# Kernel tuning notes

Measured on AMD Instinct MI355X. Metric: run time of the kernel, lower is better.

The kernel has to match this reference:

```python
import jax, jax.numpy as jnp
import numpy as np

N_GRAPHS = 64
EPS = 1e-5

def setup_inputs() -> dict:
    key = jax.random.key(0)
    ks = jax.random.split(key, 5)
    N, E, F_IN, F_OUT = 50000, 800000, 64, 64
    x = jax.random.normal(ks[0], (N, F_IN), dtype=jnp.float32)
    W = jax.random.normal(ks[1], (F_IN, F_OUT), dtype=jnp.float32) * (1.0 / np.sqrt(F_IN))
    b = jnp.zeros((F_OUT,), dtype=jnp.float32)
    gn_weight = jnp.ones((F_OUT,), dtype=jnp.float32)
    gn_bias = jnp.zeros((F_OUT,), dtype=jnp.float32)
    gn_mean_scale = jnp.ones((F_OUT,), dtype=jnp.float32)
    edge_index = jax.random.randint(ks[2], (2, E), 0, N, dtype=jnp.int64)
    batch = jnp.sort(jax.random.randint(ks[3], (N,), 0, N_GRAPHS, dtype=jnp.int64))
    return {"x": x, "W": W, "b": b, "gn_weight": gn_weight, "gn_bias": gn_bias,
            "gn_mean_scale": gn_mean_scale, "edge_index": edge_index, "batch": batch}

def reference(x, W, b, gn_weight, gn_bias, gn_mean_scale, edge_index, batch):
    N = x.shape[0]
    # --- GCNConv: add self-loops, symmetric degree normalization ---
    loop = jnp.arange(N, dtype=edge_index.dtype)
    src = jnp.concatenate([edge_index[0], loop])  # message sources (x_j)
    dst = jnp.concatenate([edge_index[1], loop])  # aggregation targets
    h = x @ W                                      # [N, F_out]
    deg = jax.ops.segment_sum(jnp.ones_like(dst, dtype=h.dtype), dst, num_segments=N)
    dinv = jnp.where(deg > 0, jax.lax.rsqrt(deg), 0.0)
    norm = dinv[src] * dinv[dst]                   # [E+N]
    out = jax.ops.segment_sum(norm[:, None] * h[src], dst, num_segments=N) + b
    # --- GraphNorm: per-graph mean/var with learnable mean scale ---
    ones = jnp.ones((N,), dtype=out.dtype)
    cnt = jax.ops.segment_sum(ones, batch, num_segments=N_GRAPHS)[:, None]  # [G,1]
    mean = jax.ops.segment_sum(out, batch, num_segments=N_GRAPHS) / cnt     # [G,F]
    centered = out - gn_mean_scale * mean[batch]
    var = jax.ops.segment_sum(centered * centered, batch, num_segments=N_GRAPHS) / cnt
    normed = centered * jax.lax.rsqrt(var[batch] + EPS)
    return jax.nn.relu(gn_weight * normed + gn_bias)
```

## Files before the change

kernel.cpp:

```cpp
#include <hip/hip_runtime.h>
#include <stdint.h>

#define EPS 1e-5f
#define NG 64
#define NP 8
#define MSLOT 64
#define CH 128

typedef float f32x4 __attribute__((ext_vector_type(4)));
typedef __bf16 bf16x8 __attribute__((ext_vector_type(8)));
typedef unsigned short u16x8 __attribute__((ext_vector_type(8)));

__device__ __forceinline__ unsigned short f2bf(float f) {
    union { float f; uint32_t u; } v; v.f = f;
    uint32_t r = v.u + 0x7fff + ((v.u >> 16) & 1);
    return (unsigned short)(r >> 16);
}
__device__ __forceinline__ float bflo(uint32_t u) {
    union { uint32_t u; float f; } v; v.u = u << 16; return v.f;
}
__device__ __forceinline__ float bfhi(uint32_t u) {
    union { uint32_t u; float f; } v; v.u = u & 0xffff0000u; return v.f;
}

__global__ __launch_bounds__(256) void setup(const float* __restrict__ W,
                                             unsigned short* __restrict__ wf,
                                             int* __restrict__ rowpos, int N,
                                             int* __restrict__ zbase, int zcount) {
    int i = blockIdx.x * 256 + threadIdx.x;
    if (i < N) rowpos[i] = i << 6;
    if (i < zcount) zbase[i] = 0;
    if (blockIdx.x == 0) {
        for (int k = threadIdx.x; k < 512; k += 256) {
            int lane = k & 63;
            int c = k >> 7;
            int s = (k >> 6) & 1;
            int col = 16 * c + (lane & 15);
            int k0 = 32 * s + (lane >> 4) * 8;
#pragma unroll
            for (int j = 0; j < 8; ++j)
                wf[k * 8 + j] = f2bf(W[(k0 + j) * 64 + col]);
        }
    }
}

__global__ __launch_bounds__(256) void fill_xcd(const int* __restrict__ src,
                                                const int* __restrict__ dst,
                                                int* __restrict__ rowpos,
                                                unsigned short* __restrict__ csr2,
                                                int E, int N, int rng, int chunk) {
    int b = blockIdx.x;
    int p = b & (NP - 1);
    int lo = p * rng;
    int hi = min(lo + rng, N);
    int base = (b >> 3) * chunk;
    int end = min(base + chunk, E);
    for (int e = base + threadIdx.x; e < end; e += 256) {
        int d = dst[e];
        if (d >= lo && d < hi) {
            int pos = atomicAdd(&rowpos[d], 1);
            if (pos < (d << 6) + MSLOT)
                __builtin_nontemporal_store((unsigned short)src[e], &csr2[pos]);
        }
    }
}

__global__ __launch_bounds__(256) void gemm_mfma(const float* __restrict__ x,
                                                 const unsigned short* __restrict__ wf,
                                                 const int* __restrict__ rowpos,
                                                 unsigned short* __restrict__ hb, int N) {
    int w = threadIdx.x >> 6;
    int lane = threadIdx.x & 63;
    int rowbase = blockIdx.x * 64 + w * 16;

    bf16x8 bfrag[4][2];
#pragma unroll
    for (int c = 0; c < 4; ++c)
#pragma unroll
        for (int s = 0; s < 2; ++s) {
            u16x8 u = *reinterpret_cast<const u16x8*>(wf + ((c * 2 + s) * 64 + lane) * 8);
            bfrag[c][s] = __builtin_bit_cast(bf16x8, u);
        }

    int ar = rowbase + (lane & 15);
    int k0 = (lane >> 4) * 8;
    bf16x8 afrag[2];
#pragma unroll
    for (int s = 0; s < 2; ++s) {
        u16x8 u = {0, 0, 0, 0, 0, 0, 0, 0};
        if (ar < N) {
            const float* xp = x + (size_t)ar * 64 + 32 * s + k0;
#pragma unroll
            for (int j = 0; j < 8; ++j) u[j] = f2bf(xp[j]);
        }
        afrag[s] = __builtin_bit_cast(bf16x8, u);
    }

    f32x4 acc[4];
#pragma unroll
    for (int c = 0; c < 4; ++c) acc[c] = (f32x4){0.f, 0.f, 0.f, 0.f};
#pragma unroll
    for (int s = 0; s < 2; ++s)
#pragma unroll
        for (int c = 0; c < 4; ++c)
            acc[c] = __builtin_amdgcn_mfma_f32_16x16x32_bf16(afrag[s], bfrag[c][s], acc[c], 0, 0, 0);

    int r0 = rowbase + (lane >> 4) * 4;
    int col = lane & 15;
#pragma unroll
    for (int j = 0; j < 4; ++j) {
        int node = r0 + j;
        if (node < N) {
            int deg = rowpos[node] - (node << 6);
            float dd = rsqrtf(1.0f + (float)deg);
#pragma unroll
            for (int c = 0; c < 4; ++c)
                hb[(size_t)node * 64 + 16 * c + col] = f2bf(acc[c][j] * dd);
        }
    }
}

__global__ __launch_bounds__(256) void gather_conv(const int* __restrict__ rowpos,
                                                   const unsigned short* __restrict__ csr2,
                                                   const uint2* __restrict__ hb2,
                                                   const float* __restrict__ bia,
                                                   float* __restrict__ out, int N) {
    int nd = blockIdx.x * 16 + (threadIdx.x >> 4);
    if (nd >= N) return;
    int l = threadIdx.x & 15;
    int degf = rowpos[nd] - (nd << 6);
    int deg = min(degf, MSLOT);
    float dd = rsqrtf(1.0f + (float)degf);

    uint2 hv = hb2[(size_t)nd * 16 + l];
    float a0 = bflo(hv.x), a1 = bfhi(hv.x), a2 = bflo(hv.y), a3 = bfhi(hv.y);
    int s0 = nd << 6;
    int s1 = s0 + deg;
    int j = s0;
    for (; j + 4 <= s1; j += 4) {
        unsigned long long iq = *reinterpret_cast<const unsigned long long*>(csr2 + j);
        int i0 = (int)(iq & 0xffff), i1 = (int)((iq >> 16) & 0xffff);
        int i2 = (int)((iq >> 32) & 0xffff), i3 = (int)(iq >> 48);
        uint2 v0 = hb2[(size_t)i0 * 16 + l];
        uint2 v1 = hb2[(size_t)i1 * 16 + l];
        uint2 v2 = hb2[(size_t)i2 * 16 + l];
        uint2 v3 = hb2[(size_t)i3 * 16 + l];
        a0 += bflo(v0.x) + bflo(v1.x) + bflo(v2.x) + bflo(v3.x);
        a1 += bfhi(v0.x) + bfhi(v1.x) + bfhi(v2.x) + bfhi(v3.x);
        a2 += bflo(v0.y) + bflo(v1.y) + bflo(v2.y) + bflo(v3.y);
        a3 += bfhi(v0.y) + bfhi(v1.y) + bfhi(v2.y) + bfhi(v3.y);
    }
    for (; j < s1; ++j) {
        uint2 v = hb2[(size_t)csr2[j] * 16 + l];
        a0 += bflo(v.x);
        a1 += bfhi(v.x);
        a2 += bflo(v.y);
        a3 += bfhi(v.y);
    }
    float4 bb = *reinterpret_cast<const float4*>(bia + 4 * l);
    float4 r;
    r.x = bb.x + dd * a0;
    r.y = bb.y + dd * a1;
    r.z = bb.z + dd * a2;
    r.w = bb.w + dd * a3;
    *reinterpret_cast<float4*>(out + (size_t)nd * 64 + 4 * l) = r;
}

__global__ __launch_bounds__(256) void stats_partial(const float* __restrict__ out,
                                                     const int* __restrict__ batch,
                                                     float* __restrict__ macc,
                                                     float* __restrict__ vacc,
                                                     int* __restrict__ cntacc, int N) {
    int c0 = blockIdx.x * CH;
    int c1 = min(c0 + CH, N);
    if (c0 >= N) return;
    int t = threadIdx.x, col = t & 63, rg = t >> 6;
    __shared__ int bsh[CH];
    __shared__ float red[4][64], red2[4][64];
    for (int i = t; i < c1 - c0; i += 256) bsh[i] = batch[c0 + i];
    __syncthreads();
    int s = c0;
    while (s < c1) {
        int g = bsh[s - c0];
        int e = s + 1;
        while (e < c1 && bsh[e - c0] == g) ++e;
        float sum = 0.f, sq = 0.f;
        for (int r = s + rg; r < e; r += 4) {
            float v = out[(size_t)r * 64 + col];
            sum += v;
            sq += v * v;
        }
        red[rg][col] = sum;
        red2[rg][col] = sq;
        __syncthreads();
        if (t < 64) {
            atomicAdd(&macc[g * 64 + t], red[0][t] + red[1][t] + red[2][t] + red[3][t]);
            atomicAdd(&vacc[g * 64 + t], red2[0][t] + red2[1][t] + red2[2][t] + red2[3][t]);
        }
        if (t == 0) atomicAdd(&cntacc[g], e - s);
        __syncthreads();
        s = e;
    }
}

__global__ void gn_final(float* __restrict__ out, const int* __restrict__ batch,
                         const float* __restrict__ ms, const float* __restrict__ macc,
                         const float* __restrict__ vacc, const int* __restrict__ cntacc,
                         const float* __restrict__ gw, const float* __restrict__ gb,
                         int total4) {
    int idx = blockIdx.x * 256 + threadIdx.x;
    if (idx >= total4) return;
    int i = idx >> 4, q = idx & 15;
    int g = batch[i];
    float inv = 1.f / (float)max(cntacc[g], 1);
    float4 mv = *reinterpret_cast<const float4*>(macc + g * 64 + 4 * q);
    float4 vv = *reinterpret_cast<const float4*>(vacc + g * 64 + 4 * q);
    float4 msf = *reinterpret_cast<const float4*>(ms + 4 * q);
    float4 gwv = *reinterpret_cast<const float4*>(gw + 4 * q);
    float4 gbv = *reinterpret_cast<const float4*>(gb + 4 * q);
    float4 o = *reinterpret_cast<const float4*>(out + (size_t)i * 64 + 4 * q);
    float m, var, y;
    float4 res;
    m = mv.x * inv; var = vv.x * inv - m * m * msf.x * (2.f - msf.x);
    y = (o.x - msf.x * m) * rsqrtf(var + EPS); res.x = fmaxf(gwv.x * y + gbv.x, 0.f);
    m = mv.y * inv; var = vv.y * inv - m * m * msf.y * (2.f - msf.y);
    y = (o.y - msf.y * m) * rsqrtf(var + EPS); res.y = fmaxf(gwv.y * y + gbv.y, 0.f);
    m = mv.z * inv; var = vv.z * inv - m * m * msf.z * (2.f - msf.z);
    y = (o.z - msf.z * m) * rsqrtf(var + EPS); res.z = fmaxf(gwv.z * y + gbv.z, 0.f);
    m = mv.w * inv; var = vv.w * inv - m * m * msf.w * (2.f - msf.w);
    y = (o.w - msf.w * m) * rsqrtf(var + EPS); res.w = fmaxf(gwv.w * y + gbv.w, 0.f);
    *reinterpret_cast<float4*>(out + (size_t)i * 64 + 4 * q) = res;
}

extern "C" void kernel_launch(void* const* d_in, const int* in_sizes, int n_in,
                              void* d_out, int out_size, void* d_ws, size_t ws_size,
                              hipStream_t stream) {
    const float* x  = (const float*)d_in[0];
    const float* W  = (const float*)d_in[1];
    const float* b  = (const float*)d_in[2];
    const float* gw = (const float*)d_in[3];
    const float* gb = (const float*)d_in[4];
    const float* ms = (const float*)d_in[5];
    const int*   edge  = (const int*)d_in[6];
    const int*   batch = (const int*)d_in[7];

    int N = in_sizes[0] / 64;
    int E = in_sizes[6] / 2;
    const int* src = edge;
    const int* dst = edge + E;

    float* out = (float*)d_out;

    unsigned short* hb = (unsigned short*)d_ws;
    int*   rowpos    = (int*)(hb + (size_t)N * 64);
    float* macc      = (float*)(rowpos + N);
    float* vacc      = macc + 64 * 64;
    int*   cntacc    = (int*)(vacc + 64 * 64);
    unsigned short* csr2 = (unsigned short*)(cntacc + 80);
    unsigned short* wf   = csr2 + (size_t)N * MSLOT;

    int chunk = (E + 255) / 256;
    int rng = (N + NP - 1) / NP;
    int zcount = 2 * 64 * 64 + 80;
    int setup_n = max(N, zcount);

    setup<<<(setup_n + 255) / 256, 256, 0, stream>>>(W, wf, rowpos, N, (int*)macc, zcount);
    fill_xcd<<<2048, 256, 0, stream>>>(src, dst, rowpos, csr2, E, N, rng, chunk);
    gemm_mfma<<<(N + 63) / 64, 256, 0, stream>>>(x, wf, rowpos, hb, N);
    gather_conv<<<(N + 15) / 16, 256, 0, stream>>>(rowpos, csr2, (const uint2*)hb, b, out, N);
    stats_partial<<<(N + CH - 1) / CH, 256, 0, stream>>>(out, batch, macc, vacc, cntacc, N);
    gn_final<<<(N * 16 + 255) / 256, 256, 0, stream>>>(out, batch, ms, macc, vacc, cntacc,
                                                       gw, gb, N * 16);
}
```

Baseline: 103.0 us.

## Split bf16 feature table into two column halves and gather each separately

The GEMM output is now written as two separate bf16 tables, each holding 32 of the 64 feature columns. The gather kernel runs over a 2D grid where blockIdx.y picks a half, using 8 lanes per node instead of 16. Each half-table is half the size of the full table, so the random neighbor gathers should hit L2/MALL more often. The cost is that the CSR index lists and degree values are read twice, and twice as many half-width row gathers are issued.

```diff
diff --git a/kernel.cpp b/kernel.cpp
--- a/kernel.cpp
+++ b/kernel.cpp
@@ -68,7 +68,8 @@
 __global__ __launch_bounds__(256) void gemm_mfma(const float* __restrict__ x,
                                                  const unsigned short* __restrict__ wf,
                                                  const int* __restrict__ rowpos,
-                                                 unsigned short* __restrict__ hb, int N) {
+                                                 unsigned short* __restrict__ hbA,
+                                                 unsigned short* __restrict__ hbB, int N) {
     int w = threadIdx.x >> 6;
     int lane = threadIdx.x & 63;
     int rowbase = blockIdx.x * 64 + w * 16;
@@ -114,25 +115,31 @@
             int deg = rowpos[node] - (node << 6);
             float dd = rsqrtf(1.0f + (float)deg);
 #pragma unroll
-            for (int c = 0; c < 4; ++c)
-                hb[(size_t)node * 64 + 16 * c + col] = f2bf(acc[c][j] * dd);
-        }
-    }
-}
-
-__global__ __launch_bounds__(256) void gather_conv(const int* __restrict__ rowpos,
+            for (int c = 0; c < 4; ++c) {
+                unsigned short v = f2bf(acc[c][j] * dd);
+                if (c < 2) hbA[(size_t)node * 32 + 16 * c + col] = v;
+                else       hbB[(size_t)node * 32 + 16 * (c - 2) + col] = v;
+            }
+        }
+    }
+}
+
+__global__ __launch_bounds__(256) void gather_half(const int* __restrict__ rowpos,
                                                    const unsigned short* __restrict__ csr2,
-                                                   const uint2* __restrict__ hb2,
+                                                   const uint2* __restrict__ hA2,
+                                                   const uint2* __restrict__ hB2,
                                                    const float* __restrict__ bia,
                                                    float* __restrict__ out, int N) {
-    int nd = blockIdx.x * 16 + (threadIdx.x >> 4);
+    int half = blockIdx.y;
+    const uint2* hb2 = half ? hB2 : hA2;
+    int nd = blockIdx.x * 32 + (threadIdx.x >> 3);
     if (nd >= N) return;
-    int l = threadIdx.x & 15;
+    int l = threadIdx.x & 7;
     int degf = rowpos[nd] - (nd << 6);
     int deg = min(degf, MSLOT);
     float dd = rsqrtf(1.0f + (float)degf);
 
-    uint2 hv = hb2[(size_t)nd * 16 + l];
+    uint2 hv = hb2[(size_t)nd * 8 + l];
     float a0 = bflo(hv.x), a1 = bfhi(hv.x), a2 = bflo(hv.y), a3 = bfhi(hv.y);
     int s0 = nd << 6;
     int s1 = s0 + deg;
@@ -141,29 +148,30 @@
         unsigned long long iq = *reinterpret_cast<const unsigned long long*>(csr2 + j);
         int i0 = (int)(iq & 0xffff), i1 = (int)((iq >> 16) & 0xffff);
         int i2 = (int)((iq >> 32) & 0xffff), i3 = (int)(iq >> 48);
-        uint2 v0 = hb2[(size_t)i0 * 16 + l];
-        uint2 v1 = hb2[(size_t)i1 * 16 + l];
-        uint2 v2 = hb2[(size_t)i2 * 16 + l];
-        uint2 v3 = hb2[(size_t)i3 * 16 + l];
+        uint2 v0 = hb2[(size_t)i0 * 8 + l];
+        uint2 v1 = hb2[(size_t)i1 * 8 + l];
+        uint2 v2 = hb2[(size_t)i2 * 8 + l];
+        uint2 v3 = hb2[(size_t)i3 * 8 + l];
         a0 += bflo(v0.x) + bflo(v1.x) + bflo(v2.x) + bflo(v3.x);
         a1 += bfhi(v0.x) + bfhi(v1.x) + bfhi(v2.x) + bfhi(v3.x);
         a2 += bflo(v0.y) + bflo(v1.y) + bflo(v2.y) + bflo(v3.y);
         a3 += bfhi(v0.y) + bfhi(v1.y) + bfhi(v2.y) + bfhi(v3.y);
     }
     for (; j < s1; ++j) {
-        uint2 v = hb2[(size_t)csr2[j] * 16 + l];
+        uint2 v = hb2[(size_t)csr2[j] * 8 + l];
         a0 += bflo(v.x);
         a1 += bfhi(v.x);
         a2 += bflo(v.y);
         a3 += bfhi(v.y);
     }
-    float4 bb = *reinterpret_cast<const float4*>(bia + 4 * l);
+    int colbase = half * 32 + 4 * l;
+    float4 bb = *reinterpret_cast<const float4*>(bia + colbase);
     float4 r;
     r.x = bb.x + dd * a0;
     r.y = bb.y + dd * a1;
     r.z = bb.z + dd * a2;
     r.w = bb.w + dd * a3;
-    *reinterpret_cast<float4*>(out + (size_t)nd * 64 + 4 * l) = r;
+    *reinterpret_cast<float4*>(out + (size_t)nd * 64 + colbase) = r;
 }
 
 __global__ __launch_bounds__(256) void stats_partial(const float* __restrict__ out,
@@ -251,8 +259,9 @@
 
     float* out = (float*)d_out;
 
-    unsigned short* hb = (unsigned short*)d_ws;
-    int*   rowpos    = (int*)(hb + (size_t)N * 64);
+    unsigned short* hbA = (unsigned short*)d_ws;
+    unsigned short* hbB = hbA + (size_t)N * 32;
+    int*   rowpos    = (int*)(hbB + (size_t)N * 32);
     float* macc      = (float*)(rowpos + N);
     float* vacc      = macc + 64 * 64;
     int*   cntacc    = (int*)(vacc + 64 * 64);
@@ -266,8 +275,9 @@
 
     setup<<<(setup_n + 255) / 256, 256, 0, stream>>>(W, wf, rowpos, N, (int*)macc, zcount);
     fill_xcd<<<2048, 256, 0, stream>>>(src, dst, rowpos, csr2, E, N, rng, chunk);
-    gemm_mfma<<<(N + 63) / 64, 256, 0, stream>>>(x, wf, rowpos, hb, N);
-    gather_conv<<<(N + 15) / 16, 256, 0, stream>>>(rowpos, csr2, (const uint2*)hb, b, out, N);
+    gemm_mfma<<<(N + 63) / 64, 256, 0, stream>>>(x, wf, rowpos, hbA, hbB, N);
+    gather_half<<<dim3((N + 31) / 32, 2), 256, 0, stream>>>(rowpos, csr2, (const uint2*)hbA,
+                                                            (const uint2*)hbB, b, out, N);
     stats_partial<<<(N + CH - 1) / CH, 256, 0, stream>>>(out, batch, macc, vacc, cntacc, N);
     gn_final<<<(N * 16 + 255) / 256, 256, 0, stream>>>(out, batch, ms, macc, vacc, cntacc,
                                                        gw, gb, N * 16);
```

Result: slower. 105.6 us (+2.6%).
